# Performance work log

Measured on AMD Instinct MI355X. Metric: run time of the kernel, lower is better.

The kernel has to match this reference:

```python
import jax, jax.numpy as jnp
import numpy as np

TOPK_RATIO = 0.2
ALIGN_WEIGHT = 1.0
REG_WEIGHT = 0.1
EPS_LN = 1e-6
EPS_COS = 1e-8


def setup_inputs() -> dict:
    key = jax.random.key(0)
    k1, k2, k3, k4, k5 = jax.random.split(key, 5)
    B, C, H, W = 8, 256, 200, 200
    return {
        "bev_map": jax.random.normal(k1, (B, C, H, W), dtype=jnp.float32),
        "prior_warp": jax.random.normal(k2, (B, C, H, W), dtype=jnp.float32),
        "dx_m": jax.random.normal(k3, (B,), dtype=jnp.float32),
        "dy_m": jax.random.normal(k4, (B,), dtype=jnp.float32),
        "dtheta": jax.random.normal(k5, (B,), dtype=jnp.float32),
    }


def _channel_layer_norm(x):
    # per-pixel mean/std over channel dim; torch std is unbiased (ddof=1)
    mu = jnp.mean(x, axis=1, keepdims=True)
    sigma = jnp.std(x, axis=1, keepdims=True, ddof=1) + EPS_LN
    return (x - mu) / sigma


def reference(bev_map, prior_warp, dx_m, dy_m, dtheta):
    B, C, H, W = bev_map.shape
    bev_norm = _channel_layer_norm(bev_map)      # [B,C,H,W]
    prior_norm = _channel_layer_norm(prior_warp)  # [B,C,H,W]

    # squared-sum score per pixel, flattened over spatial dims
    score = jnp.sum(bev_map * bev_map, axis=1).reshape(B, H * W)  # [B,HW]
    k = max(1, int(TOPK_RATIO * H * W))
    _, idx = jax.lax.top_k(score, k)             # [B,k]

    idx_bc = jnp.broadcast_to(idx[:, None, :], (B, C, k))
    bev_topk = jnp.take_along_axis(bev_norm.reshape(B, C, H * W), idx_bc, axis=2)
    prior_topk = jnp.take_along_axis(prior_norm.reshape(B, C, H * W), idx_bc, axis=2)

    # cosine similarity over channel dim (torch eps semantics: clamp each norm)
    num = jnp.sum(bev_topk * prior_topk, axis=1)                       # [B,k]
    na = jnp.sqrt(jnp.sum(bev_topk * bev_topk, axis=1))
    nb = jnp.sqrt(jnp.sum(prior_topk * prior_topk, axis=1))
    sim = num / (jnp.maximum(na, EPS_COS) * jnp.maximum(nb, EPS_COS))
    align_loss = jnp.mean(1.0 - sim)

    reg_loss = jnp.mean(dx_m * dx_m + dy_m * dy_m) + jnp.mean(dtheta * dtheta)
    return ALIGN_WEIGHT * align_loss + REG_WEIGHT * reg_loss
```

## Files before the change

### kernel.cpp

```cpp
#include <hip/hip_runtime.h>
#include <math.h>

#define BATCH 8
#define CCH 256
#define HW 40000
#define HW4 (HW / 4)
#define KSEL 8000
#define EPS_LN 1e-6f
#define EPS_COS 1e-8f

#define OFF_KEYS    0
#define OFF_CONTRIB 320000
#define OFF_HIST1   640000
#define OFF_BSUMS   1164288

typedef float v4f __attribute__((ext_vector_type(4)));
#define NT(p) __builtin_nontemporal_load(p)

__device__ __forceinline__ unsigned int mono_key(float x) {
  unsigned int u = __float_as_uint(x);
  return (u & 0x80000000u) ? ~u : (u | 0x80000000u);
}

__global__ __launch_bounds__(256) void zero_kernel(unsigned int* __restrict__ ws) {
  const int n4 = (BATCH * 65536) / 4;
  uint4* p = (uint4*)(ws + OFF_HIST1);
  uint4 z = {0u, 0u, 0u, 0u};
  for (int i = blockIdx.x * blockDim.x + threadIdx.x; i < n4; i += gridDim.x * blockDim.x)
    p[i] = z;
  if (blockIdx.x == 0 && threadIdx.x < BATCH) ws[OFF_BSUMS + threadIdx.x] = 0u;
}

__global__ __launch_bounds__(256, 1) void pixel_stats_kernel(
    const float* __restrict__ A, const float* __restrict__ B,
    unsigned int* __restrict__ keys, float* __restrict__ contrib,
    unsigned int* __restrict__ ws) {
  int tid = blockIdx.x * blockDim.x + threadIdx.x;
  if (tid >= BATCH * HW4) return;
  int b = tid / HW4;
  int p4 = tid - b * HW4;
  const v4f* a  = (const v4f*)(A + (size_t)b * CCH * HW) + p4;
  const v4f* bb = (const v4f*)(B + (size_t)b * CCH * HW) + p4;

  float sa[4] = {0, 0, 0, 0}, ssa[4] = {0, 0, 0, 0};
  float sb[4] = {0, 0, 0, 0}, ssb[4] = {0, 0, 0, 0}, dab[4] = {0, 0, 0, 0};

  v4f xA[8], yA[8], xB[8], yB[8];
#pragma unroll
  for (int k = 0; k < 8; ++k) {
    xA[k] = NT(a + (size_t)k * HW4);
    yA[k] = NT(bb + (size_t)k * HW4);
  }

#pragma unroll 1
  for (int it = 0; it < 16; ++it) {
    const size_t cb = (size_t)it * 16;
#pragma unroll
    for (int k = 0; k < 8; ++k) {
      xB[k] = NT(a + (cb + 8 + (size_t)k) * HW4);
      yB[k] = NT(bb + (cb + 8 + (size_t)k) * HW4);
    }
#pragma unroll
    for (int k = 0; k < 8; ++k) {
#pragma unroll
      for (int j = 0; j < 4; ++j) {
        float xs = xA[k][j], ys = yA[k][j];
        sa[j] += xs;  ssa[j] = fmaf(xs, xs, ssa[j]);
        sb[j] += ys;  ssb[j] = fmaf(ys, ys, ssb[j]);
        dab[j] = fmaf(xs, ys, dab[j]);
      }
    }
    if (it < 15) {
#pragma unroll
      for (int k = 0; k < 8; ++k) {
        xA[k] = NT(a + (cb + 16 + (size_t)k) * HW4);
        yA[k] = NT(bb + (cb + 16 + (size_t)k) * HW4);
      }
    }
#pragma unroll
    for (int k = 0; k < 8; ++k) {
#pragma unroll
      for (int j = 0; j < 4; ++j) {
        float xs = xB[k][j], ys = yB[k][j];
        sa[j] += xs;  ssa[j] = fmaf(xs, xs, ssa[j]);
        sb[j] += ys;  ssb[j] = fmaf(ys, ys, ssb[j]);
        dab[j] = fmaf(xs, ys, dab[j]);
      }
    }
  }

  unsigned int kv[4];
  float cov[4];
  const float invC = 1.0f / (float)CCH;
#pragma unroll
  for (int j = 0; j < 4; ++j) {
    kv[j] = mono_key(ssa[j]);
    float mua = sa[j] * invC, mub = sb[j] * invC;
    float cssa = fmaxf(ssa[j] - (float)CCH * mua * mua, 0.f);
    float cssb = fmaxf(ssb[j] - (float)CCH * mub * mub, 0.f);
    float cdot = dab[j] - (float)CCH * mua * mub;
    float siga = sqrtf(cssa / (float)(CCH - 1)) + EPS_LN;
    float sigb = sqrtf(cssb / (float)(CCH - 1)) + EPS_LN;
    float num = cdot / (siga * sigb);
    float na = sqrtf(cssa) / siga;
    float nb = sqrtf(cssb) / sigb;
    cov[j] = 1.0f - num / (fmaxf(na, EPS_COS) * fmaxf(nb, EPS_COS));
  }
  int out = b * HW + p4 * 4;
  *(uint4*)(keys + out)  = make_uint4(kv[0], kv[1], kv[2], kv[3]);
  *(v4f*)(contrib + out) = (v4f){cov[0], cov[1], cov[2], cov[3]};

  unsigned int* h1 = ws + OFF_HIST1 + (b << 16);
#pragma unroll
  for (int j = 0; j < 4; ++j)
    atomicAdd(&h1[kv[j] >> 16], 1u);
}

__global__ __launch_bounds__(1024) void select_sum_kernel(
    const unsigned int* __restrict__ keys, const float* __restrict__ contrib,
    unsigned int* __restrict__ ws) {
  int b = blockIdx.x;
  int t = threadIdx.x;
  const unsigned int* kb = keys + b * HW;
  const float* cbp = contrib + b * HW;

  __shared__ unsigned int suf[1024];
  __shared__ unsigned int bins[64];
  __shared__ unsigned int hbin[256];
  __shared__ unsigned int s_idx, s_above;
  __shared__ unsigned int s_tie;

  unsigned int prefix, K;

  {
    const unsigned int* h = ws + OFF_HIST1 + (b << 16);
    unsigned int sum = 0;
#pragma unroll 8
    for (int i = 0; i < 64; ++i) sum += h[t * 64 + i];
    suf[t] = sum;
    __syncthreads();
    for (int off = 1; off < 1024; off <<= 1) {
      unsigned int v = (t + off < 1024) ? suf[t + off] : 0u;
      __syncthreads();
      suf[t] += v;
      __syncthreads();
    }
    unsigned int above = (t == 1023) ? 0u : suf[t + 1];
    if (suf[t] >= (unsigned)KSEL && above < (unsigned)KSEL) { s_idx = (unsigned)t; s_above = above; }
    __syncthreads();
    if (t < 64) bins[t] = h[s_idx * 64 + t];
    __syncthreads();
    if (t == 0) {
      unsigned int cum = s_above;
      int d = 63;
      for (; d >= 0; --d) {
        if (cum + bins[d] >= (unsigned)KSEL) break;
        cum += bins[d];
      }
      s_idx = s_idx * 64 + (unsigned)d;
      s_above = cum;
    }
    __syncthreads();
    prefix = s_idx;
    K = (unsigned)KSEL - s_above;
    __syncthreads();
  }

#pragma unroll 1
  for (int pass = 0; pass < 2; ++pass) {
    if (t < 256) hbin[t] = 0u;
    __syncthreads();
    if (pass == 0) {
      for (int i = t; i < HW; i += 1024) {
        unsigned int key = kb[i];
        if ((key >> 16) == prefix) atomicAdd(&hbin[(key >> 8) & 0xFFu], 1u);
      }
    } else {
      for (int i = t; i < HW; i += 1024) {
        unsigned int key = kb[i];
        if ((key >> 8) == prefix) atomicAdd(&hbin[key & 0xFFu], 1u);
      }
    }
    __syncthreads();
    if (t < 256) suf[t] = hbin[t];
    __syncthreads();
    for (int off = 1; off < 256; off <<= 1) {
      unsigned int v = (t < 256 && t + off < 256) ? suf[t + off] : 0u;
      __syncthreads();
      if (t < 256) suf[t] += v;
      __syncthreads();
    }
    if (t < 256) {
      unsigned int above = (t == 255) ? 0u : suf[t + 1];
      if (suf[t] >= K && above < K) { s_idx = (unsigned)t; s_above = above; }
    }
    __syncthreads();
    prefix = (prefix << 8) | s_idx;
    K = K - s_above;
    __syncthreads();
  }

  const unsigned int T = prefix;
  const unsigned int rem2 = K;
  if (t == 0) s_tie = 0u;
  __syncthreads();

  float partial = 0.f;
  for (int i = t; i < HW; i += 1024) {
    unsigned int key = kb[i];
    if (key > T) {
      partial += cbp[i];
    } else if (key == T) {
      unsigned int old = atomicAdd(&s_tie, 1u);
      if (old < rem2) partial += cbp[i];
    }
  }
  __syncthreads();
  float* redf = (float*)suf;
  redf[t] = partial;
  __syncthreads();
  for (int off = 512; off > 0; off >>= 1) {
    if (t < off) redf[t] += redf[t + off];
    __syncthreads();
  }
  if (t == 0) ((float*)(ws + OFF_BSUMS))[b] = redf[0];
}

__global__ void finalize_kernel(const unsigned int* __restrict__ ws,
                                const float* __restrict__ dx,
                                const float* __restrict__ dy,
                                const float* __restrict__ dth,
                                float* __restrict__ out) {
  if (threadIdx.x == 0 && blockIdx.x == 0) {
    const float* bsums = (const float*)(ws + OFF_BSUMS);
    float s = 0.f;
    for (int b = 0; b < BATCH; ++b) s += bsums[b];
    float align = s / (float)(BATCH * KSEL);
    float r1 = 0.f, r2 = 0.f;
    for (int b = 0; b < BATCH; ++b) {
      r1 += dx[b] * dx[b] + dy[b] * dy[b];
      r2 += dth[b] * dth[b];
    }
    out[0] = align + 0.1f * (r1 / (float)BATCH + r2 / (float)BATCH);
  }
}

extern "C" void kernel_launch(void* const* d_in, const int* in_sizes, int n_in,
                              void* d_out, int out_size, void* d_ws, size_t ws_size,
                              hipStream_t stream) {
  const float* bev   = (const float*)d_in[0];
  const float* prior = (const float*)d_in[1];
  const float* dx    = (const float*)d_in[2];
  const float* dy    = (const float*)d_in[3];
  const float* dth   = (const float*)d_in[4];
  float* out = (float*)d_out;

  unsigned int* ws = (unsigned int*)d_ws;
  unsigned int* keys = ws + OFF_KEYS;
  float* contrib     = (float*)ws + OFF_CONTRIB;

  zero_kernel<<<256, 256, 0, stream>>>(ws);
  pixel_stats_kernel<<<(BATCH * HW4 + 255) / 256, 256, 0, stream>>>(bev, prior, keys, contrib, ws);
  select_sum_kernel<<<BATCH, 1024, 0, stream>>>(keys, contrib, ws);
  finalize_kernel<<<1, 64, 0, stream>>>(ws, dx, dy, dth, out);
}
```

Before: 733.9 us.

## Halve per-thread pixel width, drop nontemporal loads, cache radix candidates in LDS

```diff
diff --git a/kernel.cpp b/kernel.cpp
--- a/kernel.cpp
+++ b/kernel.cpp
@@ -4,18 +4,18 @@
 #define BATCH 8
 #define CCH 256
 #define HW 40000
-#define HW4 (HW / 4)
+#define HW2 (HW / 2)
 #define KSEL 8000
 #define EPS_LN 1e-6f
 #define EPS_COS 1e-8f
+#define CAP 16384
 
 #define OFF_KEYS    0
 #define OFF_CONTRIB 320000
 #define OFF_HIST1   640000
 #define OFF_BSUMS   1164288
 
-typedef float v4f __attribute__((ext_vector_type(4)));
-#define NT(p) __builtin_nontemporal_load(p)
+typedef float v2f __attribute__((ext_vector_type(2)));
 
 __device__ __forceinline__ unsigned int mono_key(float x) {
   unsigned int u = __float_as_uint(x);
@@ -31,25 +31,25 @@
   if (blockIdx.x == 0 && threadIdx.x < BATCH) ws[OFF_BSUMS + threadIdx.x] = 0u;
 }
 
-__global__ __launch_bounds__(256, 1) void pixel_stats_kernel(
+__global__ __launch_bounds__(256, 2) void pixel_stats_kernel(
     const float* __restrict__ A, const float* __restrict__ B,
     unsigned int* __restrict__ keys, float* __restrict__ contrib,
     unsigned int* __restrict__ ws) {
   int tid = blockIdx.x * blockDim.x + threadIdx.x;
-  if (tid >= BATCH * HW4) return;
-  int b = tid / HW4;
-  int p4 = tid - b * HW4;
-  const v4f* a  = (const v4f*)(A + (size_t)b * CCH * HW) + p4;
-  const v4f* bb = (const v4f*)(B + (size_t)b * CCH * HW) + p4;
-
-  float sa[4] = {0, 0, 0, 0}, ssa[4] = {0, 0, 0, 0};
-  float sb[4] = {0, 0, 0, 0}, ssb[4] = {0, 0, 0, 0}, dab[4] = {0, 0, 0, 0};
-
-  v4f xA[8], yA[8], xB[8], yB[8];
+  if (tid >= BATCH * HW2) return;
+  int b = tid / HW2;
+  int p2 = tid - b * HW2;
+  const v2f* a  = (const v2f*)(A + (size_t)b * CCH * HW) + p2;
+  const v2f* bb = (const v2f*)(B + (size_t)b * CCH * HW) + p2;
+
+  float sa[2] = {0, 0}, ssa[2] = {0, 0};
+  float sb[2] = {0, 0}, ssb[2] = {0, 0}, dab[2] = {0, 0};
+
+  v2f xA[8], yA[8], xB[8], yB[8];
 #pragma unroll
   for (int k = 0; k < 8; ++k) {
-    xA[k] = NT(a + (size_t)k * HW4);
-    yA[k] = NT(bb + (size_t)k * HW4);
+    xA[k] = a[(size_t)k * HW2];
+    yA[k] = bb[(size_t)k * HW2];
   }
 
 #pragma unroll 1
@@ -57,13 +57,13 @@
     const size_t cb = (size_t)it * 16;
 #pragma unroll
     for (int k = 0; k < 8; ++k) {
-      xB[k] = NT(a + (cb + 8 + (size_t)k) * HW4);
-      yB[k] = NT(bb + (cb + 8 + (size_t)k) * HW4);
+      xB[k] = a[(cb + 8 + (size_t)k) * HW2];
+      yB[k] = bb[(cb + 8 + (size_t)k) * HW2];
     }
 #pragma unroll
     for (int k = 0; k < 8; ++k) {
 #pragma unroll
-      for (int j = 0; j < 4; ++j) {
+      for (int j = 0; j < 2; ++j) {
         float xs = xA[k][j], ys = yA[k][j];
         sa[j] += xs;  ssa[j] = fmaf(xs, xs, ssa[j]);
         sb[j] += ys;  ssb[j] = fmaf(ys, ys, ssb[j]);
@@ -73,14 +73,14 @@
     if (it < 15) {
 #pragma unroll
       for (int k = 0; k < 8; ++k) {
-        xA[k] = NT(a + (cb + 16 + (size_t)k) * HW4);
-        yA[k] = NT(bb + (cb + 16 + (size_t)k) * HW4);
+        xA[k] = a[(cb + 16 + (size_t)k) * HW2];
+        yA[k] = bb[(cb + 16 + (size_t)k) * HW2];
       }
     }
 #pragma unroll
     for (int k = 0; k < 8; ++k) {
 #pragma unroll
-      for (int j = 0; j < 4; ++j) {
+      for (int j = 0; j < 2; ++j) {
         float xs = xB[k][j], ys = yB[k][j];
         sa[j] += xs;  ssa[j] = fmaf(xs, xs, ssa[j]);
         sb[j] += ys;  ssb[j] = fmaf(ys, ys, ssb[j]);
@@ -89,11 +89,11 @@
     }
   }
 
-  unsigned int kv[4];
-  float cov[4];
+  unsigned int kv[2];
+  float cov[2];
   const float invC = 1.0f / (float)CCH;
 #pragma unroll
-  for (int j = 0; j < 4; ++j) {
+  for (int j = 0; j < 2; ++j) {
     kv[j] = mono_key(ssa[j]);
     float mua = sa[j] * invC, mub = sb[j] * invC;
     float cssa = fmaxf(ssa[j] - (float)CCH * mua * mua, 0.f);
@@ -106,13 +106,13 @@
     float nb = sqrtf(cssb) / sigb;
     cov[j] = 1.0f - num / (fmaxf(na, EPS_COS) * fmaxf(nb, EPS_COS));
   }
-  int out = b * HW + p4 * 4;
-  *(uint4*)(keys + out)  = make_uint4(kv[0], kv[1], kv[2], kv[3]);
-  *(v4f*)(contrib + out) = (v4f){cov[0], cov[1], cov[2], cov[3]};
+  int out = b * HW + p2 * 2;
+  *(uint2*)(keys + out)  = make_uint2(kv[0], kv[1]);
+  *(v2f*)(contrib + out) = (v2f){cov[0], cov[1]};
 
   unsigned int* h1 = ws + OFF_HIST1 + (b << 16);
 #pragma unroll
-  for (int j = 0; j < 4; ++j)
+  for (int j = 0; j < 2; ++j)
     atomicAdd(&h1[kv[j] >> 16], 1u);
 }
 
@@ -127,8 +127,9 @@
   __shared__ unsigned int suf[1024];
   __shared__ unsigned int bins[64];
   __shared__ unsigned int hbin[256];
-  __shared__ unsigned int s_idx, s_above;
-  __shared__ unsigned int s_tie;
+  __shared__ unsigned int s_idx, s_above, s_tie, s_cnt;
+  __shared__ unsigned int lds_k[CAP];
+  __shared__ float lds_c[CAP];
 
   unsigned int prefix, K;
 
@@ -166,21 +167,26 @@
     __syncthreads();
   }
 
-#pragma unroll 1
-  for (int pass = 0; pass < 2; ++pass) {
+  if (t == 0) s_cnt = 0u;
+  __syncthreads();
+  float partial = 0.f;
+  for (int i = t; i < HW; i += 1024) {
+    unsigned int key = kb[i];
+    unsigned int h16 = key >> 16;
+    if (h16 > prefix) {
+      partial += cbp[i];
+    } else if (h16 == prefix) {
+      unsigned int c = atomicAdd(&s_cnt, 1u);
+      if (c < CAP) { lds_k[c] = key & 0xFFFFu; lds_c[c] = cbp[i]; }
+    }
+  }
+  __syncthreads();
+  const unsigned int M = s_cnt;
+
+  if (M <= CAP) {
     if (t < 256) hbin[t] = 0u;
     __syncthreads();
-    if (pass == 0) {
-      for (int i = t; i < HW; i += 1024) {
-        unsigned int key = kb[i];
-        if ((key >> 16) == prefix) atomicAdd(&hbin[(key >> 8) & 0xFFu], 1u);
-      }
-    } else {
-      for (int i = t; i < HW; i += 1024) {
-        unsigned int key = kb[i];
-        if ((key >> 8) == prefix) atomicAdd(&hbin[key & 0xFFu], 1u);
-      }
-    }
+    for (int i = t; i < (int)M; i += 1024) atomicAdd(&hbin[lds_k[i] >> 8], 1u);
     __syncthreads();
     if (t < 256) suf[t] = hbin[t];
     __syncthreads();
@@ -195,26 +201,92 @@
       if (suf[t] >= K && above < K) { s_idx = (unsigned)t; s_above = above; }
     }
     __syncthreads();
-    prefix = (prefix << 8) | s_idx;
-    K = K - s_above;
-    __syncthreads();
-  }
-
-  const unsigned int T = prefix;
-  const unsigned int rem2 = K;
-  if (t == 0) s_tie = 0u;
-  __syncthreads();
-
-  float partial = 0.f;
-  for (int i = t; i < HW; i += 1024) {
-    unsigned int key = kb[i];
-    if (key > T) {
-      partial += cbp[i];
-    } else if (key == T) {
-      unsigned int old = atomicAdd(&s_tie, 1u);
-      if (old < rem2) partial += cbp[i];
-    }
-  }
+    const unsigned int byte1 = s_idx;
+    K -= s_above;
+    __syncthreads();
+    if (t < 256) hbin[t] = 0u;
+    __syncthreads();
+    for (int i = t; i < (int)M; i += 1024) {
+      unsigned int lk = lds_k[i];
+      if ((lk >> 8) == byte1) atomicAdd(&hbin[lk & 0xFFu], 1u);
+    }
+    __syncthreads();
+    if (t < 256) suf[t] = hbin[t];
+    __syncthreads();
+    for (int off = 1; off < 256; off <<= 1) {
+      unsigned int v = (t < 256 && t + off < 256) ? suf[t + off] : 0u;
+      __syncthreads();
+      if (t < 256) suf[t] += v;
+      __syncthreads();
+    }
+    if (t < 256) {
+      unsigned int above = (t == 255) ? 0u : suf[t + 1];
+      if (suf[t] >= K && above < K) { s_idx = (unsigned)t; s_above = above; }
+    }
+    __syncthreads();
+    const unsigned int Tlow = (byte1 << 8) | s_idx;
+    const unsigned int rem = K - s_above;
+    if (t == 0) s_tie = 0u;
+    __syncthreads();
+    for (int i = t; i < (int)M; i += 1024) {
+      unsigned int lk = lds_k[i];
+      if (lk > Tlow) {
+        partial += lds_c[i];
+      } else if (lk == Tlow) {
+        unsigned int old = atomicAdd(&s_tie, 1u);
+        if (old < rem) partial += lds_c[i];
+      }
+    }
+  } else {
+    partial = 0.f;
+#pragma unroll 1
+    for (int pass = 0; pass < 2; ++pass) {
+      if (t < 256) hbin[t] = 0u;
+      __syncthreads();
+      if (pass == 0) {
+        for (int i = t; i < HW; i += 1024) {
+          unsigned int key = kb[i];
+          if ((key >> 16) == prefix) atomicAdd(&hbin[(key >> 8) & 0xFFu], 1u);
+        }
+      } else {
+        for (int i = t; i < HW; i += 1024) {
+          unsigned int key = kb[i];
+          if ((key >> 8) == prefix) atomicAdd(&hbin[key & 0xFFu], 1u);
+        }
+      }
+      __syncthreads();
+      if (t < 256) suf[t] = hbin[t];
+      __syncthreads();
+      for (int off = 1; off < 256; off <<= 1) {
+        unsigned int v = (t < 256 && t + off < 256) ? suf[t + off] : 0u;
+        __syncthreads();
+        if (t < 256) suf[t] += v;
+        __syncthreads();
+      }
+      if (t < 256) {
+        unsigned int above = (t == 255) ? 0u : suf[t + 1];
+        if (suf[t] >= K && above < K) { s_idx = (unsigned)t; s_above = above; }
+      }
+      __syncthreads();
+      prefix = (prefix << 8) | s_idx;
+      K = K - s_above;
+      __syncthreads();
+    }
+    const unsigned int T = prefix;
+    const unsigned int rem2 = K;
+    if (t == 0) s_tie = 0u;
+    __syncthreads();
+    for (int i = t; i < HW; i += 1024) {
+      unsigned int key = kb[i];
+      if (key > T) {
+        partial += cbp[i];
+      } else if (key == T) {
+        unsigned int old = atomicAdd(&s_tie, 1u);
+        if (old < rem2) partial += cbp[i];
+      }
+    }
+  }
+
   __syncthreads();
   float* redf = (float*)suf;
   redf[t] = partial;
@@ -260,7 +332,7 @@
   float* contrib     = (float*)ws + OFF_CONTRIB;
 
   zero_kernel<<<256, 256, 0, stream>>>(ws);
-  pixel_stats_kernel<<<(BATCH * HW4 + 255) / 256, 256, 0, stream>>>(bev, prior, keys, contrib, ws);
+  pixel_stats_kernel<<<(BATCH * HW2 + 255) / 256, 256, 0, stream>>>(bev, prior, keys, contrib, ws);
   select_sum_kernel<<<BATCH, 1024, 0, stream>>>(keys, contrib, ws);
   finalize_kernel<<<1, 64, 0, stream>>>(ws, dx, dy, dth, out);
 }
```

Result: slower. 750.9 us (+2.3%).
